# Kernel tuning notes

Measured on AMD Instinct MI355X. Metric: run time of the kernel, lower is better.

Reference implementation:

```python
import jax, jax.numpy as jnp
import numpy as np

N = 100000   # nodes
E = 3200000  # edges
M = 4096     # moves
K = 16       # orders per move
NEG_SLOPE = 0.2  # PyG GATv2Conv default negative_slope

PARAM_SHAPES = {
    'g1_Wl': (10, 15), 'g1_Wr': (10, 15), 'g1_att': (10,), 'g1_b': (10,),
    'g2_Wl': (10, 25), 'g2_Wr': (10, 25), 'g2_att': (10,), 'g2_b': (10,),
    'g3_Wl': (10, 25), 'g3_Wr': (10, 25), 'g3_att': (10,), 'g3_b': (10,),
    'vt_W': (20, 29), 'vt_b': (20,), 'va_W': (1, 20), 'va_b': (1,),
    'vv_W': (10, 20), 'vv_b': (10,), 'vl_W': (1, 10), 'vl_b': (1,),
    'at_W': (20, 48), 'at_b': (20,), 'dt_W': (20, 23), 'dt_b': (20,),
    'oa_W': (1, 20), 'oa_b': (1,), 'ov_W': (1, 20), 'ov_b': (1,),
}
PARAM_NAMES = list(PARAM_SHAPES.keys())


def _linear(x, W, b):
    return x @ W.T + b


def _gatv2(x, src, dst, Wl, Wr, att, b):
    # GATv2Conv (heads=1, self-loops appended by caller), eval mode (no dropout)
    xl = x @ Wl.T  # messages from source nodes
    xr = x @ Wr.T
    e = (jax.nn.leaky_relu(xl[src] + xr[dst], NEG_SLOPE) * att).sum(-1)  # [E+N]
    emax = jax.ops.segment_max(e, dst, num_segments=N)
    ee = jnp.exp(e - emax[dst])
    denom = jax.ops.segment_sum(ee, dst, num_segments=N)
    alpha = ee / denom[dst]
    return jax.ops.segment_sum(alpha[:, None] * xl[src], dst, num_segments=N) + b


def _forward(x1, x2, edges, move_src, move_dst, move_armies, is_attack, params):
    (g1_Wl, g1_Wr, g1_att, g1_b,
     g2_Wl, g2_Wr, g2_att, g2_b,
     g3_Wl, g3_Wr, g3_att, g3_b,
     vt_W, vt_b, va_W, va_b, vv_W, vv_b, vl_W, vl_b,
     at_W, at_b, dt_W, dt_b, oa_W, oa_b, ov_W, ov_b) = params
    x2t = jnp.tile(x2, (N, 1))  # [N,4]
    self_idx = jnp.arange(N, dtype=edges.dtype)
    src = jnp.concatenate([edges[0], self_idx])
    dst = jnp.concatenate([edges[1], self_idx])
    x = jax.nn.relu(_gatv2(x1, src, dst, g1_Wl, g1_Wr, g1_att, g1_b))
    x = jax.nn.relu(_gatv2(jnp.concatenate([x, x1], 1), src, dst, g2_Wl, g2_Wr, g2_att, g2_b))
    x = jax.nn.relu(_gatv2(jnp.concatenate([x, x1], 1), src, dst, g3_Wl, g3_Wr, g3_att, g3_b))  # [N,10]
    # per-move order tensors (vectorized over [M,K]); deploy uses move_src as target
    xs, xd = x[move_src], x[move_dst]       # [M,K,10]
    x1s, x1d = x1[move_src], x1[move_dst]   # [M,K,15]
    extra = 0.6 * move_armies - 0.7 * (x1d[..., 3] + x1d[..., 4])
    attack_in = jnp.concatenate([xs, xd, x1s[..., 3:], x1d[..., 1:],
                                 move_armies[..., None], extra[..., None]], -1)  # [M,K,48]
    deploy_in = jnp.concatenate([xs, x1s[..., 3:], move_armies[..., None]], -1)  # [M,K,23]
    feat = jnp.where(is_attack[..., None] == 1,
                     _linear(attack_in, at_W, at_b),
                     _linear(deploy_in, dt_W, dt_b))
    feat = jax.nn.relu(feat)  # dropout = identity (eval)
    attn = jax.nn.softmax(_linear(feat, oa_W, oa_b), axis=1)  # softmax over orders
    p = (attn * _linear(feat, ov_W, ov_b)).sum(axis=(1, 2))   # [M]
    # value head: attention pooling over all nodes
    Vn = jax.nn.relu(_linear(jnp.concatenate([x, x1, x2t], 1), vt_W, vt_b))  # [N,20]
    vatt = jax.nn.softmax(_linear(Vn, va_W, va_b), axis=0)
    Vp = jax.nn.relu((vatt * _linear(Vn, vv_W, vv_b)).sum(axis=0))
    V = jnp.tanh(_linear(Vp, vl_W, vl_b))[0]
    return V, jax.nn.log_softmax(p, axis=0)


def setup_inputs() -> dict:
    key = jax.random.key(0)
    ks = iter(jax.random.split(key, 64))
    inp = {
        'x1': jax.random.normal(next(ks), (N, 15), jnp.float32),
        'x2': jax.random.normal(next(ks), (4,), jnp.float32),
        'edges': jax.random.randint(next(ks), (2, E), 0, N, jnp.int32),
        'move_src': jax.random.randint(next(ks), (M, K), 0, N, jnp.int32),
        'move_dst': jax.random.randint(next(ks), (M, K), 0, N, jnp.int32),
        'move_armies': jax.random.uniform(next(ks), (M, K), jnp.float32) * 10.0,
        'is_attack': jax.random.randint(next(ks), (M, K), 0, 2, jnp.int32),
    }
    for name, shape in PARAM_SHAPES.items():
        inp[name] = jax.random.normal(next(ks), shape, jnp.float32) * 0.1
    return inp


def reference(x1, x2, edges, move_src, move_dst, move_armies, is_attack,
              g1_Wl, g1_Wr, g1_att, g1_b, g2_Wl, g2_Wr, g2_att, g2_b,
              g3_Wl, g3_Wr, g3_att, g3_b, vt_W, vt_b, va_W, va_b,
              vv_W, vv_b, vl_W, vl_b, at_W, at_b, dt_W, dt_b,
              oa_W, oa_b, ov_W, ov_b):
    params = (g1_Wl, g1_Wr, g1_att, g1_b, g2_Wl, g2_Wr, g2_att, g2_b,
              g3_Wl, g3_Wr, g3_att, g3_b, vt_W, vt_b, va_W, va_b,
              vv_W, vv_b, vl_W, vl_b, at_W, at_b, dt_W, dt_b,
              oa_W, oa_b, ov_W, ov_b)
    return _forward(x1, x2, edges, move_src, move_dst, move_armies, is_attack, params)
```

## Files before the change

### kernel.cpp

```cpp
#include <hip/hip_runtime.h>
#include <hip/hip_fp16.h>
#include <math.h>

#define NN 100000
#define NE 3200000
#define MM 4096
#define KK 16
#define NEG_SLOPE 0.2f
#define SUB 8
#define BSH 8
#define NB 391
#define PCH 4096
#define FCAP 9728
#define XS 12
#define XSU 4
#define PART_BLOCKS ((NE + NN + PCH - 1) / PCH)
#define LIN_BLOCKS  ((NN + 255) / 256)
#define MOVE_BLOCKS ((MM * KK) / 256)
#define VAL_BLOCKS  ((NN + 255) / 256)
#define CSTR 16
#define PZ ((int)0xAAAAAAAAu)

typedef float vfloat2 __attribute__((__vector_size__(2 * sizeof(float))));

__device__ __forceinline__ void f8x10_decode(const uint4& w, float* xs) {
    vfloat2 f0 = __builtin_amdgcn_cvt_pk_f32_fp8(w.x, false); xs[0]=f0[0]; xs[1]=f0[1];
    vfloat2 f1 = __builtin_amdgcn_cvt_pk_f32_fp8(w.x, true);  xs[2]=f1[0]; xs[3]=f1[1];
    vfloat2 f2 = __builtin_amdgcn_cvt_pk_f32_fp8(w.y, false); xs[4]=f2[0]; xs[5]=f2[1];
    vfloat2 f3 = __builtin_amdgcn_cvt_pk_f32_fp8(w.y, true);  xs[6]=f3[0]; xs[7]=f3[1];
    vfloat2 f4 = __builtin_amdgcn_cvt_pk_f32_fp8(w.z, false); xs[8]=f4[0]; xs[9]=f4[1];
}
__device__ __forceinline__ uint4 f8x10_encode(const float* v) {
    unsigned u0 = __builtin_amdgcn_cvt_pk_fp8_f32(v[0], v[1], 0, false);
    u0 = __builtin_amdgcn_cvt_pk_fp8_f32(v[2], v[3], u0, true);
    unsigned u1 = __builtin_amdgcn_cvt_pk_fp8_f32(v[4], v[5], 0, false);
    u1 = __builtin_amdgcn_cvt_pk_fp8_f32(v[6], v[7], u1, true);
    unsigned u2 = __builtin_amdgcn_cvt_pk_fp8_f32(v[8], v[9], 0, false);
    return make_uint4(u0, u1, u2, 0u);
}

__global__ __launch_bounds__(256) void part_lin1_kernel(const int* __restrict__ edges,
                                                        int* __restrict__ cnt,
                                                        unsigned* __restrict__ recs,
                                                        const float* __restrict__ x1,
                                                        const float* __restrict__ Wl,
                                                        const float* __restrict__ Wr,
                                                        unsigned* __restrict__ xl8,
                                                        float* __restrict__ xr) {
    int t = threadIdx.x;
    if (blockIdx.x >= PART_BLOCKS) {
        int i = (blockIdx.x - PART_BLOCKS) * 256 + t;
        if (i >= NN) return;
        float in[15];
        #pragma unroll
        for (int j = 0; j < 15; j++) in[j] = x1[(long)i * 15 + j];
        float sl[10];
        #pragma unroll
        for (int o = 0; o < 10; o++) {
            float l = 0.f, r = 0.f;
            #pragma unroll
            for (int j = 0; j < 15; j++) {
                l += Wl[o * 15 + j] * in[j];
                r += Wr[o * 15 + j] * in[j];
            }
            sl[o] = l;
            xr[(long)i * XS + o] = r;
        }
        *(uint4*)(xl8 + (long)i * XSU) = f8x10_encode(sl);
        return;
    }
    __shared__ unsigned rl[PCH];
    __shared__ unsigned short bb[PCH];
    __shared__ int h[NB];
    __shared__ int gb[NB];
    __shared__ int cur[NB];
    const int total = NE + NN;
    int base = blockIdx.x * PCH;
    int n = min(PCH, total - base);
    for (int b = t; b < NB; b += 256) { h[b] = 0; cur[b] = 0; }
    __syncthreads();
    for (int j = t; j < n; j += 256) {
        int i = base + j;
        int s, d;
        if (i < NE) { s = edges[i]; d = edges[NE + i]; }
        else        { s = i - NE; d = s; }
        rl[j] = ((unsigned)(d & 255) << 17) | (unsigned)s;
        int b = d >> BSH;
        bb[j] = (unsigned short)b;
        atomicAdd(&h[b], 1);
    }
    __syncthreads();
    for (int b = t; b < NB; b += 256) {
        int hv = h[b];
        if (hv > 0) gb[b] = atomicAdd(&cnt[b * CSTR], hv) - PZ;
    }
    __syncthreads();
    for (int j = t; j < n; j += 256) {
        int b = bb[j];
        int l = atomicAdd(&cur[b], 1);
        int pos = gb[b] + l;
        if (pos >= 0 && pos < FCAP) recs[(long)b * FCAP + pos] = rl[j];
    }
}

__global__ __launch_bounds__(1024) void fine_sort_kernel(const unsigned* __restrict__ recs,
                                                         const int* __restrict__ cnt,
                                                         int* __restrict__ csr_src,
                                                         int* __restrict__ offsets) {
    __shared__ unsigned rl[FCAP];
    __shared__ int scn[512];
    __shared__ int hist[256];
    __shared__ int sc[256];
    __shared__ int hb[257];
    __shared__ int cur[256];
    int b = blockIdx.x;
    int t = threadIdx.x;
    int c = 0;
    if (t < 512) {
        c = (t < NB) ? min(max(cnt[t * CSTR] - PZ, 0), FCAP) : 0;
        scn[t] = c;
    }
    __syncthreads();
    for (int off = 1; off < 512; off <<= 1) {
        int v = 0;
        if (t < 512 && t >= off) v = scn[t - off];
        __syncthreads();
        if (t < 512) scn[t] += v;
        __syncthreads();
    }
    int beg = (b == 0) ? 0 : scn[b - 1];
    int nb = min(max(cnt[b * CSTR] - PZ, 0), FCAP);
    int nodebase = b << BSH;
    int nnodes = min(256, NN - nodebase);
    if (t < 256) { hist[t] = 0; cur[t] = 0; }
    __syncthreads();
    const unsigned* rsrc = recs + (long)b * FCAP;
    for (int j = t; j < nb; j += 1024) {
        unsigned r = rsrc[j];
        rl[j] = r;
        atomicAdd(&hist[r >> 17], 1);
    }
    __syncthreads();
    int hv = (t < 256) ? hist[t] : 0;
    if (t < 256) sc[t] = hv;
    __syncthreads();
    for (int off = 1; off < 256; off <<= 1) {
        int v = 0;
        if (t < 256 && t >= off) v = sc[t - off];
        __syncthreads();
        if (t < 256) sc[t] += v;
        __syncthreads();
    }
    if (t < 256) hb[t] = sc[t] - hv;
    if (t == 0) hb[256] = nb;
    __syncthreads();
    for (int j = t; j < nb; j += 1024) {
        unsigned r = rl[j];
        int l = r >> 17;
        int p = hb[l] + atomicAdd(&cur[l], 1);
        csr_src[beg + p] = (int)(r & 0x1FFFFu);
    }
    if (t < nnodes) offsets[nodebase + t] = beg + hb[t];
    if (b == NB - 1 && t == 0) offsets[NN] = beg + nb;
}

template<bool FUSE_NEXT>
__global__ void gat_aggregate_kernel(const int* __restrict__ csr_src,
                                     const int* __restrict__ offsets,
                                     const unsigned* __restrict__ xl8,
                                     const float* __restrict__ xr,
                                     const float* __restrict__ att,
                                     const float* __restrict__ b,
                                     const float* __restrict__ x1,
                                     const float* __restrict__ nWl,
                                     const float* __restrict__ nWr,
                                     unsigned* __restrict__ xlo,
                                     float* __restrict__ xro,
                                     float* __restrict__ xout)
{
    int t = blockIdx.x * blockDim.x + threadIdx.x;
    int node = t / SUB;
    int lane = t % SUB;
    if (node >= NN) return;
    float xrn[12], a[10];
    const float4* xr4 = (const float4*)(xr + (long)node * XS);
    #pragma unroll
    for (int q = 0; q < 3; q++) {
        float4 v = xr4[q];
        xrn[4*q] = v.x; xrn[4*q+1] = v.y; xrn[4*q+2] = v.z; xrn[4*q+3] = v.w;
    }
    #pragma unroll
    for (int h = 0; h < 10; h++) a[h] = att[h];
    int beg = offsets[node], end = offsets[node + 1];
    float den = 0.f, num[10];
    #pragma unroll
    for (int h = 0; h < 10; h++) num[h] = 0.f;
    int j = beg + lane;
    for (; j + 3 * SUB < end; j += 4 * SUB) {
        int s0 = csr_src[j];
        int s1 = csr_src[j + SUB];
        int s2 = csr_src[j + 2 * SUB];
        int s3 = csr_src[j + 3 * SUB];
        uint4 wa[4];
        wa[0] = *(const uint4*)(xl8 + (long)s0 * XSU);
        wa[1] = *(const uint4*)(xl8 + (long)s1 * XSU);
        wa[2] = *(const uint4*)(xl8 + (long)s2 * XSU);
        wa[3] = *(const uint4*)(xl8 + (long)s3 * XSU);
        #pragma unroll
        for (int q = 0; q < 4; q++) {
            float xs[10];
            f8x10_decode(wa[q], xs);
            float e = 0.f;
            #pragma unroll
            for (int h = 0; h < 10; h++) {
                float v = xs[h] + xrn[h];
                v = (v >= 0.f) ? v : NEG_SLOPE * v;
                e += v * a[h];
            }
            float w = __expf(e);
            den += w;
            #pragma unroll
            for (int h = 0; h < 10; h++) num[h] += w * xs[h];
        }
    }
    for (; j < end; j += SUB) {
        int s = csr_src[j];
        uint4 wa = *(const uint4*)(xl8 + (long)s * XSU);
        float xs[10];
        f8x10_decode(wa, xs);
        float e = 0.f;
        #pragma unroll
        for (int h = 0; h < 10; h++) {
            float v = xs[h] + xrn[h];
            v = (v >= 0.f) ? v : NEG_SLOPE * v;
            e += v * a[h];
        }
        float w = __expf(e);
        den += w;
        #pragma unroll
        for (int h = 0; h < 10; h++) num[h] += w * xs[h];
    }
    #pragma unroll
    for (int off = SUB / 2; off; off >>= 1) {
        den += __shfl_xor(den, off, SUB);
        #pragma unroll
        for (int h = 0; h < 10; h++) num[h] += __shfl_xor(num[h], off, SUB);
    }
    float inv = 1.f / den;
    float xo[10];
    #pragma unroll
    for (int h = 0; h < 10; h++) xo[h] = fmaxf(num[h] * inv + b[h], 0.f);
    if (FUSE_NEXT) {
        if (lane < 5) {
            float in2[25];
            #pragma unroll
            for (int h = 0; h < 10; h++) in2[h] = xo[h];
            #pragma unroll
            for (int h = 0; h < 15; h++) in2[10 + h] = x1[(long)node * 15 + h];
            int o0 = 2 * lane, o1 = 2 * lane + 1;
            float sl0 = 0.f, sl1 = 0.f, sr0 = 0.f, sr1 = 0.f;
            #pragma unroll
            for (int jj = 0; jj < 25; jj++) {
                sl0 += nWl[o0 * 25 + jj] * in2[jj];
                sl1 += nWl[o1 * 25 + jj] * in2[jj];
                sr0 += nWr[o0 * 25 + jj] * in2[jj];
                sr1 += nWr[o1 * 25 + jj] * in2[jj];
            }
            unsigned pk = __builtin_amdgcn_cvt_pk_fp8_f32(sl0, sl1, 0, false);
            ((unsigned short*)(xlo + (long)node * XSU))[lane] = (unsigned short)pk;
            *(float2*)(xro + (long)node * XS + o0) = make_float2(sr0, sr1);
        }
    } else {
        if (lane == 0) {
            #pragma unroll
            for (int h = 0; h < 10; h++) xout[(long)node * XS + h] = xo[h];
        }
    }
}

__global__ void move_value_kernel(const float* __restrict__ x,
                                  const float* __restrict__ x1,
                                  const float* __restrict__ x2,
                                  const int* __restrict__ msrc,
                                  const int* __restrict__ mdst,
                                  const float* __restrict__ armies,
                                  const int* __restrict__ isatk,
                                  const float* __restrict__ at_W, const float* __restrict__ at_b,
                                  const float* __restrict__ dt_W, const float* __restrict__ dt_b,
                                  const float* __restrict__ oa_W, const float* __restrict__ oa_b,
                                  const float* __restrict__ ov_W, const float* __restrict__ ov_b,
                                  const float* __restrict__ vt_W, const float* __restrict__ vt_b,
                                  const float* __restrict__ va_W, const float* __restrict__ va_b,
                                  const float* __restrict__ vv_W, const float* __restrict__ vv_b,
                                  float* __restrict__ p,
                                  float* __restrict__ partials) {
    if (blockIdx.x < MOVE_BLOCKS) {
        int t = blockIdx.x * 256 + threadIdx.x;
        int m = t >> 4;
        int k = t & 15;
        int s = msrc[t], d = mdst[t];
        float arm = armies[t];
        bool atk = (isatk[t] == 1);
        float xsrc[12];
        const float4* xs4 = (const float4*)(x + (long)s * XS);
        #pragma unroll
        for (int q = 0; q < 3; q++) {
            float4 v = xs4[q];
            xsrc[4*q]=v.x; xsrc[4*q+1]=v.y; xsrc[4*q+2]=v.z; xsrc[4*q+3]=v.w;
        }
        float feat[20];
        if (atk) {
            float in[48];
            #pragma unroll
            for (int h = 0; h < 10; h++) in[h] = xsrc[h];
            const float4* xd4 = (const float4*)(x + (long)d * XS);
            float xdst[12];
            #pragma unroll
            for (int q = 0; q < 3; q++) {
                float4 v = xd4[q];
                xdst[4*q]=v.x; xdst[4*q+1]=v.y; xdst[4*q+2]=v.z; xdst[4*q+3]=v.w;
            }
            #pragma unroll
            for (int h = 0; h < 10; h++) in[10 + h] = xdst[h];
            #pragma unroll
            for (int h = 0; h < 12; h++) in[20 + h] = x1[(long)s * 15 + 3 + h];
            #pragma unroll
            for (int h = 0; h < 14; h++) in[32 + h] = x1[(long)d * 15 + 1 + h];
            in[46] = arm;
            in[47] = 0.6f * arm - 0.7f * (x1[(long)d * 15 + 3] + x1[(long)d * 15 + 4]);
            #pragma unroll
            for (int o = 0; o < 20; o++) {
                float sum = at_b[o];
                #pragma unroll
                for (int j = 0; j < 48; j++) sum += at_W[o * 48 + j] * in[j];
                feat[o] = fmaxf(sum, 0.f);
            }
        } else {
            float in[23];
            #pragma unroll
            for (int h = 0; h < 10; h++) in[h] = xsrc[h];
            #pragma unroll
            for (int h = 0; h < 12; h++) in[10 + h] = x1[(long)s * 15 + 3 + h];
            in[22] = arm;
            #pragma unroll
            for (int o = 0; o < 20; o++) {
                float sum = dt_b[o];
                #pragma unroll
                for (int j = 0; j < 23; j++) sum += dt_W[o * 23 + j] * in[j];
                feat[o] = fmaxf(sum, 0.f);
            }
        }
        float oa = oa_b[0], ov = ov_b[0];
        #pragma unroll
        for (int j = 0; j < 20; j++) {
            oa += oa_W[j] * feat[j];
            ov += ov_W[j] * feat[j];
        }
        float mx = oa;
        #pragma unroll
        for (int off = 8; off; off >>= 1) mx = fmaxf(mx, __shfl_xor(mx, off, 16));
        float w = __expf(oa - mx);
        float nume = w * ov;
        float den = w;
        #pragma unroll
        for (int off = 8; off; off >>= 1) {
            nume += __shfl_xor(nume, off, 16);
            den  += __shfl_xor(den,  off, 16);
        }
        if (k == 0) p[m] = nume / den;
        return;
    }
    __shared__ float sm[4][11];
    int vb = blockIdx.x - MOVE_BLOCKS;
    int i = vb * 256 + threadIdx.x;
    float w = 0.f;
    float acc[10];
    #pragma unroll
    for (int h = 0; h < 10; h++) acc[h] = 0.f;
    if (i < NN) {
        float in[29];
        const float4* xi4 = (const float4*)(x + (long)i * XS);
        float xi[12];
        #pragma unroll
        for (int q = 0; q < 3; q++) {
            float4 v = xi4[q];
            xi[4*q]=v.x; xi[4*q+1]=v.y; xi[4*q+2]=v.z; xi[4*q+3]=v.w;
        }
        #pragma unroll
        for (int h = 0; h < 10; h++) in[h] = xi[h];
        #pragma unroll
        for (int h = 0; h < 15; h++) in[10 + h] = x1[(long)i * 15 + h];
        #pragma unroll
        for (int h = 0; h < 4; h++) in[25 + h] = x2[h];
        float Vn[20];
        #pragma unroll
        for (int o = 0; o < 20; o++) {
            float s = vt_b[o];
            #pragma unroll
            for (int j = 0; j < 29; j++) s += vt_W[o * 29 + j] * in[j];
            Vn[o] = fmaxf(s, 0.f);
        }
        float lg = va_b[0];
        #pragma unroll
        for (int j = 0; j < 20; j++) lg += va_W[j] * Vn[j];
        w = __expf(lg);
        #pragma unroll
        for (int o = 0; o < 10; o++) {
            float s = vv_b[o];
            #pragma unroll
            for (int j = 0; j < 20; j++) s += vv_W[o * 20 + j] * Vn[j];
            acc[o] = w * s;
        }
    }
    #pragma unroll
    for (int off = 32; off; off >>= 1) {
        w += __shfl_xor(w, off, 64);
        #pragma unroll
        for (int h = 0; h < 10; h++) acc[h] += __shfl_xor(acc[h], off, 64);
    }
    int wid = threadIdx.x >> 6;
    if ((threadIdx.x & 63) == 0) {
        #pragma unroll
        for (int h = 0; h < 10; h++) sm[wid][h] = acc[h];
        sm[wid][10] = w;
    }
    __syncthreads();
    if (threadIdx.x < 11) {
        int c = threadIdx.x;
        partials[(long)vb * 12 + c] = sm[0][c] + sm[1][c] + sm[2][c] + sm[3][c];
    }
}

__global__ void final_kernel(const float* __restrict__ p,
                             const float* __restrict__ partials,
                             const float* __restrict__ vl_W, const float* __restrict__ vl_b,
                             float* __restrict__ out) {
    if (blockIdx.x == 0) {
        __shared__ float sm[256];
        int tid = threadIdx.x;
        float mx = -INFINITY;
        for (int i = tid; i < MM; i += 256) mx = fmaxf(mx, p[i]);
        sm[tid] = mx; __syncthreads();
        for (int s = 128; s; s >>= 1) { if (tid < s) sm[tid] = fmaxf(sm[tid], sm[tid + s]); __syncthreads(); }
        mx = sm[0]; __syncthreads();
        float sum = 0.f;
        for (int i = tid; i < MM; i += 256) sum += expf(p[i] - mx);
        sm[tid] = sum; __syncthreads();
        for (int s = 128; s; s >>= 1) { if (tid < s) sm[tid] += sm[tid + s]; __syncthreads(); }
        float ls = mx + logf(sm[0]);
        for (int i = tid; i < MM; i += 256) out[1 + i] = p[i] - ls;
    } else if (threadIdx.x < 64) {
        int lane = threadIdx.x;
        float s[11];
        #pragma unroll
        for (int c = 0; c < 11; c++) s[c] = 0.f;
        for (int j = lane; j < VAL_BLOCKS; j += 64)
            #pragma unroll
            for (int c = 0; c < 11; c++) s[c] += partials[(long)j * 12 + c];
        #pragma unroll
        for (int off = 32; off; off >>= 1)
            #pragma unroll
            for (int c = 0; c < 11; c++) s[c] += __shfl_xor(s[c], off, 64);
        if (lane == 0) {
            float inv = 1.0f / s[10];
            float v = vl_b[0];
            #pragma unroll
            for (int h = 0; h < 10; h++) v += vl_W[h] * fmaxf(s[h] * inv, 0.f);
            out[0] = tanhf(v);
        }
    }
}

extern "C" void kernel_launch(void* const* d_in, const int* in_sizes, int n_in,
                              void* d_out, int out_size, void* d_ws, size_t ws_size,
                              hipStream_t stream) {
    const float* x1      = (const float*)d_in[0];
    const float* x2      = (const float*)d_in[1];
    const int*   edges   = (const int*)d_in[2];
    const int*   msrc    = (const int*)d_in[3];
    const int*   mdst    = (const int*)d_in[4];
    const float* armies  = (const float*)d_in[5];
    const int*   isatk   = (const int*)d_in[6];
    const float* g1_Wl = (const float*)d_in[7],  *g1_Wr = (const float*)d_in[8];
    const float* g1_att= (const float*)d_in[9],  *g1_b  = (const float*)d_in[10];
    const float* g2_Wl = (const float*)d_in[11], *g2_Wr = (const float*)d_in[12];
    const float* g2_att= (const float*)d_in[13], *g2_b  = (const float*)d_in[14];
    const float* g3_Wl = (const float*)d_in[15], *g3_Wr = (const float*)d_in[16];
    const float* g3_att= (const float*)d_in[17], *g3_b  = (const float*)d_in[18];
    const float* vt_W  = (const float*)d_in[19], *vt_b  = (const float*)d_in[20];
    const float* va_W  = (const float*)d_in[21], *va_b  = (const float*)d_in[22];
    const float* vv_W  = (const float*)d_in[23], *vv_b  = (const float*)d_in[24];
    const float* vl_W  = (const float*)d_in[25], *vl_b  = (const float*)d_in[26];
    const float* at_W  = (const float*)d_in[27], *at_b  = (const float*)d_in[28];
    const float* dt_W  = (const float*)d_in[29], *dt_b  = (const float*)d_in[30];
    const float* oa_W  = (const float*)d_in[31], *oa_b  = (const float*)d_in[32];
    const float* ov_W  = (const float*)d_in[33], *ov_b  = (const float*)d_in[34];

    float* out = (float*)d_out;

    float* ws = (float*)d_ws;
    unsigned* xl8A = (unsigned*)ws;
    unsigned* xl8B = xl8A + (long)NN * XSU;
    float* xrA = (float*)(xl8B + (long)NN * XSU);
    float* xrB = xrA + (long)NN * XS;
    float* xF  = xrB + (long)NN * XS;
    int* csr_src = (int*)(xF + (long)NN * XS);
    int* offsets = csr_src + (NE + NN);
    unsigned* recs = (unsigned*)(offsets + NN + 4);
    int* cnt   = (int*)(recs + (long)NB * FCAP);
    float* pbuf = (float*)(cnt + NB * CSTR + 16);
    float* partials = pbuf + MM;

    const int aggBlocks = ((long)NN * SUB + 255) / 256;

    part_lin1_kernel<<<PART_BLOCKS + LIN_BLOCKS, 256, 0, stream>>>(
        edges, cnt, recs, x1, g1_Wl, g1_Wr, xl8A, xrA);
    fine_sort_kernel<<<NB, 1024, 0, stream>>>(recs, cnt, csr_src, offsets);
    gat_aggregate_kernel<true><<<aggBlocks, 256, 0, stream>>>(
        csr_src, offsets, xl8A, xrA, g1_att, g1_b, x1, g2_Wl, g2_Wr, xl8B, xrB, nullptr);
    gat_aggregate_kernel<true><<<aggBlocks, 256, 0, stream>>>(
        csr_src, offsets, xl8B, xrB, g2_att, g2_b, x1, g3_Wl, g3_Wr, xl8A, xrA, nullptr);
    gat_aggregate_kernel<false><<<aggBlocks, 256, 0, stream>>>(
        csr_src, offsets, xl8A, xrA, g3_att, g3_b, x1, nullptr, nullptr, nullptr, nullptr, xF);
    move_value_kernel<<<MOVE_BLOCKS + VAL_BLOCKS, 256, 0, stream>>>(
        xF, x1, x2, msrc, mdst, armies, isatk,
        at_W, at_b, dt_W, dt_b, oa_W, oa_b, ov_W, ov_b,
        vt_W, vt_b, va_W, va_b, vv_W, vv_b, pbuf, partials);
    final_kernel<<<2, 256, 0, stream>>>(pbuf, partials, vl_W, vl_b, out);
}
```

Before: 334.8 us.

## Split coarse bucket partition into count, scan, and scatter kernels

Replaces the single-pass partition, which claimed bucket slots with global atomics and staged records in shared memory, with three kernels: a per-chunk histogram, a per-bucket scan over chunk histograms, and a scatter that re-reads edges and writes records at deterministic offsets. This removes global atomic contention on the bucket counters and the large shared-memory staging, which should raise occupancy. In exchange the edge array is read twice and two extra launches are added. The chunk size is doubled and the histogram buffer reuses the csr_src region.

```diff
diff --git a/kernel.cpp b/kernel.cpp
--- a/kernel.cpp
+++ b/kernel.cpp
@@ -10,11 +10,11 @@
 #define SUB 8
 #define BSH 8
 #define NB 391
-#define PCH 4096
+#define PCH 8192
 #define FCAP 9728
 #define XS 12
 #define XSU 4
-#define PART_BLOCKS ((NE + NN + PCH - 1) / PCH)
+#define CNT_BLOCKS ((NE + NN + PCH - 1) / PCH)
 #define LIN_BLOCKS  ((NN + 255) / 256)
 #define MOVE_BLOCKS ((MM * KK) / 256)
 #define VAL_BLOCKS  ((NN + 255) / 256)
@@ -40,16 +40,15 @@
 }
 
 __global__ __launch_bounds__(256) void part_lin1_kernel(const int* __restrict__ edges,
-                                                        int* __restrict__ cnt,
-                                                        unsigned* __restrict__ recs,
+                                                        int* __restrict__ hist,
                                                         const float* __restrict__ x1,
                                                         const float* __restrict__ Wl,
                                                         const float* __restrict__ Wr,
                                                         unsigned* __restrict__ xl8,
                                                         float* __restrict__ xr) {
     int t = threadIdx.x;
-    if (blockIdx.x >= PART_BLOCKS) {
-        int i = (blockIdx.x - PART_BLOCKS) * 256 + t;
+    if (blockIdx.x >= CNT_BLOCKS) {
+        int i = (blockIdx.x - CNT_BLOCKS) * 256 + t;
         if (i >= NN) return;
         float in[15];
         #pragma unroll
@@ -69,37 +68,65 @@
         *(uint4*)(xl8 + (long)i * XSU) = f8x10_encode(sl);
         return;
     }
-    __shared__ unsigned rl[PCH];
-    __shared__ unsigned short bb[PCH];
     __shared__ int h[NB];
-    __shared__ int gb[NB];
-    __shared__ int cur[NB];
     const int total = NE + NN;
     int base = blockIdx.x * PCH;
     int n = min(PCH, total - base);
-    for (int b = t; b < NB; b += 256) { h[b] = 0; cur[b] = 0; }
+    for (int b = t; b < NB; b += 256) h[b] = 0;
+    __syncthreads();
+    for (int j = t; j < n; j += 256) {
+        int i = base + j;
+        int d = (i < NE) ? edges[NE + i] : (i - NE);
+        atomicAdd(&h[d >> BSH], 1);
+    }
+    __syncthreads();
+    for (int b = t; b < NB; b += 256) hist[blockIdx.x * NB + b] = h[b];
+}
+
+__global__ __launch_bounds__(64) void scan_kernel(int* __restrict__ hist,
+                                                  int* __restrict__ cnt) {
+    int b = blockIdx.x;
+    int lane = threadIdx.x;
+    int base = 0;
+    const int chunks = (CNT_BLOCKS + 63) / 64;
+    for (int c = 0; c < chunks; c++) {
+        int idx = c * 64 + lane;
+        int v = (idx < CNT_BLOCKS) ? hist[idx * NB + b] : 0;
+        int x = v;
+        #pragma unroll
+        for (int off = 1; off < 64; off <<= 1) {
+            int y = __shfl_up(x, off, 64);
+            if (lane >= off) x += y;
+        }
+        if (idx < CNT_BLOCKS) hist[idx * NB + b] = base + x - v;
+        base += __shfl(x, 63, 64);
+    }
+    if (lane == 0) cnt[b * CSTR] = base + PZ;
+}
+
+__global__ __launch_bounds__(256) void scatter_kernel(const int* __restrict__ edges,
+                                                      const int* __restrict__ hist,
+                                                      unsigned* __restrict__ recs) {
+    __shared__ int gb[NB];
+    __shared__ int cur[NB];
+    int t = threadIdx.x;
+    const int total = NE + NN;
+    int base = blockIdx.x * PCH;
+    int n = min(PCH, total - base);
+    for (int b = t; b < NB; b += 256) {
+        gb[b] = hist[blockIdx.x * NB + b];
+        cur[b] = 0;
+    }
     __syncthreads();
     for (int j = t; j < n; j += 256) {
         int i = base + j;
         int s, d;
         if (i < NE) { s = edges[i]; d = edges[NE + i]; }
         else        { s = i - NE; d = s; }
-        rl[j] = ((unsigned)(d & 255) << 17) | (unsigned)s;
         int b = d >> BSH;
-        bb[j] = (unsigned short)b;
-        atomicAdd(&h[b], 1);
-    }
-    __syncthreads();
-    for (int b = t; b < NB; b += 256) {
-        int hv = h[b];
-        if (hv > 0) gb[b] = atomicAdd(&cnt[b * CSTR], hv) - PZ;
-    }
-    __syncthreads();
-    for (int j = t; j < n; j += 256) {
-        int b = bb[j];
         int l = atomicAdd(&cur[b], 1);
         int pos = gb[b] + l;
-        if (pos >= 0 && pos < FCAP) recs[(long)b * FCAP + pos] = rl[j];
+        if (pos < FCAP) recs[(long)b * FCAP + pos] = ((unsigned)(d & 255) << 17) | (unsigned)s;
     }
 }
 
@@ -510,11 +537,14 @@
     int* cnt   = (int*)(recs + (long)NB * FCAP);
     float* pbuf = (float*)(cnt + NB * CSTR + 16);
     float* partials = pbuf + MM;
+    int* hist = csr_src;
 
     const int aggBlocks = ((long)NN * SUB + 255) / 256;
 
-    part_lin1_kernel<<<PART_BLOCKS + LIN_BLOCKS, 256, 0, stream>>>(
-        edges, cnt, recs, x1, g1_Wl, g1_Wr, xl8A, xrA);
+    part_lin1_kernel<<<CNT_BLOCKS + LIN_BLOCKS, 256, 0, stream>>>(
+        edges, hist, x1, g1_Wl, g1_Wr, xl8A, xrA);
+    scan_kernel<<<NB, 64, 0, stream>>>(hist, cnt);
+    scatter_kernel<<<CNT_BLOCKS, 256, 0, stream>>>(edges, hist, recs);
     fine_sort_kernel<<<NB, 1024, 0, stream>>>(recs, cnt, csr_src, offsets);
     gat_aggregate_kernel<true><<<aggBlocks, 256, 0, stream>>>(
         csr_src, offsets, xl8A, xrA, g1_att, g1_b, x1, g2_Wl, g2_Wr, xl8B, xrB, nullptr);
```

Result: slower. 344.9 us (+3.0%).

## Replace two-level bucket sort CSR build with global histogram, scan, atomic scatter

Applied to the files above, without the earlier changes.

Builds the destination-sorted CSR with a global per-node atomic histogram, a two-kernel prefix scan and an atomic-cursor scatter of sources. This replaces the coarse bucket partition plus shared-memory fine sort. The goal is to drop the intermediate record buffer and the large-LDS fine-sort kernel. In exchange it adds two extra launches and many global atomics on random destinations. Within a node the edge order becomes nondeterministic, which may change floating-point summation order.

```diff
diff --git a/kernel.cpp b/kernel.cpp
--- a/kernel.cpp
+++ b/kernel.cpp
@@ -8,17 +8,14 @@
 #define KK 16
 #define NEG_SLOPE 0.2f
 #define SUB 8
-#define BSH 8
 #define NB 391
-#define PCH 4096
-#define FCAP 9728
 #define XS 12
 #define XSU 4
-#define PART_BLOCKS ((NE + NN + PCH - 1) / PCH)
+#define HIST_BLOCKS 512
 #define LIN_BLOCKS  ((NN + 255) / 256)
+#define SC_BLOCKS   1024
 #define MOVE_BLOCKS ((MM * KK) / 256)
 #define VAL_BLOCKS  ((NN + 255) / 256)
-#define CSTR 16
 #define PZ ((int)0xAAAAAAAAu)
 
 typedef float vfloat2 __attribute__((__vector_size__(2 * sizeof(float))));
@@ -40,16 +37,15 @@
 }
 
 __global__ __launch_bounds__(256) void part_lin1_kernel(const int* __restrict__ edges,
-                                                        int* __restrict__ cnt,
-                                                        unsigned* __restrict__ recs,
+                                                        int* __restrict__ ghist,
                                                         const float* __restrict__ x1,
                                                         const float* __restrict__ Wl,
                                                         const float* __restrict__ Wr,
                                                         unsigned* __restrict__ xl8,
                                                         float* __restrict__ xr) {
     int t = threadIdx.x;
-    if (blockIdx.x >= PART_BLOCKS) {
-        int i = (blockIdx.x - PART_BLOCKS) * 256 + t;
+    if (blockIdx.x >= HIST_BLOCKS) {
+        int i = (blockIdx.x - HIST_BLOCKS) * 256 + t;
         if (i >= NN) return;
         float in[15];
         #pragma unroll
@@ -69,99 +65,87 @@
         *(uint4*)(xl8 + (long)i * XSU) = f8x10_encode(sl);
         return;
     }
-    __shared__ unsigned rl[PCH];
-    __shared__ unsigned short bb[PCH];
-    __shared__ int h[NB];
-    __shared__ int gb[NB];
-    __shared__ int cur[NB];
-    const int total = NE + NN;
-    int base = blockIdx.x * PCH;
-    int n = min(PCH, total - base);
-    for (int b = t; b < NB; b += 256) { h[b] = 0; cur[b] = 0; }
+    long gid = (long)blockIdx.x * 256 + t;
+    const long stride = (long)HIST_BLOCKS * 256;
+    for (long i = gid; i < NE; i += stride)
+        atomicAdd(&ghist[edges[NE + i]], 1);
+}
+
+__global__ __launch_bounds__(256) void scan1_kernel(const int* __restrict__ ghist,
+                                                    int* __restrict__ chunkTot) {
+    int c = blockIdx.x, t = threadIdx.x;
+    int i = c * 256 + t;
+    int w = (i < NN) ? (ghist[i] - PZ + 1) : 0;
+    #pragma unroll
+    for (int off = 32; off; off >>= 1) w += __shfl_xor(w, off, 64);
+    __shared__ int rb[4];
+    if ((t & 63) == 0) rb[t >> 6] = w;
     __syncthreads();
-    for (int j = t; j < n; j += 256) {
-        int i = base + j;
-        int s, d;
-        if (i < NE) { s = edges[i]; d = edges[NE + i]; }
-        else        { s = i - NE; d = s; }
-        rl[j] = ((unsigned)(d & 255) << 17) | (unsigned)s;
-        int b = d >> BSH;
-        bb[j] = (unsigned short)b;
-        atomicAdd(&h[b], 1);
-    }
+    if (t == 0) chunkTot[c] = rb[0] + rb[1] + rb[2] + rb[3];
+}
+
+__global__ __launch_bounds__(256) void scan2_kernel(const int* __restrict__ ghist,
+                                                    const int* __restrict__ chunkTot,
+                                                    int* __restrict__ offsets,
+                                                    int* __restrict__ cur,
+                                                    int* __restrict__ csr_src) {
+    __shared__ int sTot[NB];
+    __shared__ int rb[4];
+    __shared__ int wt[4];
+    int c = blockIdx.x, t = threadIdx.x;
+    int lane = t & 63, wid = t >> 6;
+    for (int j = t; j < NB; j += 256) sTot[j] = chunkTot[j];
     __syncthreads();
-    for (int b = t; b < NB; b += 256) {
-        int hv = h[b];
-        if (hv > 0) gb[b] = atomicAdd(&cnt[b * CSTR], hv) - PZ;
-    }
+    int part = 0;
+    for (int j = t; j < c; j += 256) part += sTot[j];
+    #pragma unroll
+    for (int off = 32; off; off >>= 1) part += __shfl_xor(part, off, 64);
+    if (lane == 0) rb[wid] = part;
     __syncthreads();
-    for (int j = t; j < n; j += 256) {
-        int b = bb[j];
-        int l = atomicAdd(&cur[b], 1);
-        int pos = gb[b] + l;
-        if (pos >= 0 && pos < FCAP) recs[(long)b * FCAP + pos] = rl[j];
-    }
-}
-
-__global__ __launch_bounds__(1024) void fine_sort_kernel(const unsigned* __restrict__ recs,
-                                                         const int* __restrict__ cnt,
-                                                         int* __restrict__ csr_src,
-                                                         int* __restrict__ offsets) {
-    __shared__ unsigned rl[FCAP];
-    __shared__ int scn[512];
-    __shared__ int hist[256];
-    __shared__ int sc[256];
-    __shared__ int hb[257];
-    __shared__ int cur[256];
-    int b = blockIdx.x;
-    int t = threadIdx.x;
-    int c = 0;
-    if (t < 512) {
-        c = (t < NB) ? min(max(cnt[t * CSTR] - PZ, 0), FCAP) : 0;
-        scn[t] = c;
-    }
+    int base = rb[0] + rb[1] + rb[2] + rb[3];
+    int i = c * 256 + t;
+    int w = (i < NN) ? (ghist[i] - PZ + 1) : 0;
+    int x = w;
+    #pragma unroll
+    for (int off = 1; off < 64; off <<= 1) {
+        int y = __shfl_up(x, off, 64);
+        if (lane >= off) x += y;
+    }
+    if (lane == 63) wt[wid] = x;
     __syncthreads();
-    for (int off = 1; off < 512; off <<= 1) {
-        int v = 0;
-        if (t < 512 && t >= off) v = scn[t - off];
-        __syncthreads();
-        if (t < 512) scn[t] += v;
-        __syncthreads();
-    }
-    int beg = (b == 0) ? 0 : scn[b - 1];
-    int nb = min(max(cnt[b * CSTR] - PZ, 0), FCAP);
-    int nodebase = b << BSH;
-    int nnodes = min(256, NN - nodebase);
-    if (t < 256) { hist[t] = 0; cur[t] = 0; }
-    __syncthreads();
-    const unsigned* rsrc = recs + (long)b * FCAP;
-    for (int j = t; j < nb; j += 1024) {
-        unsigned r = rsrc[j];
-        rl[j] = r;
-        atomicAdd(&hist[r >> 17], 1);
-    }
-    __syncthreads();
-    int hv = (t < 256) ? hist[t] : 0;
-    if (t < 256) sc[t] = hv;
-    __syncthreads();
-    for (int off = 1; off < 256; off <<= 1) {
-        int v = 0;
-        if (t < 256 && t >= off) v = sc[t - off];
-        __syncthreads();
-        if (t < 256) sc[t] += v;
-        __syncthreads();
-    }
-    if (t < 256) hb[t] = sc[t] - hv;
-    if (t == 0) hb[256] = nb;
-    __syncthreads();
-    for (int j = t; j < nb; j += 1024) {
-        unsigned r = rl[j];
-        int l = r >> 17;
-        int p = hb[l] + atomicAdd(&cur[l], 1);
-        csr_src[beg + p] = (int)(r & 0x1FFFFu);
-    }
-    if (t < nnodes) offsets[nodebase + t] = beg + hb[t];
-    if (b == NB - 1 && t == 0) offsets[NN] = beg + nb;
+    int wb = 0;
+    for (int q = 0; q < wid; q++) wb += wt[q];
+    int endp = base + wb + x;
+    if (i < NN) {
+        int beg = endp - w;
+        offsets[i] = beg;
+        cur[i] = beg;
+        csr_src[endp - 1] = i;
+        if (i == NN - 1) offsets[NN] = endp;
+    }
+}
+
+__global__ __launch_bounds__(256) void scatter_kernel(const int* __restrict__ edges,
+                                                      int* __restrict__ cur,
+                                                      int* __restrict__ csr_src) {
+    long gid = (long)blockIdx.x * 256 + threadIdx.x;
+    const long stride = (long)SC_BLOCKS * 256;
+    for (long i0 = gid; i0 < NE; i0 += 4 * stride) {
+        int ss[4], dd[4], pp[4];
+        bool vl[4];
+        #pragma unroll
+        for (int q = 0; q < 4; q++) {
+            long i = i0 + q * stride;
+            vl[q] = (i < NE);
+            if (vl[q]) { ss[q] = edges[i]; dd[q] = edges[NE + i]; }
+        }
+        #pragma unroll
+        for (int q = 0; q < 4; q++)
+            if (vl[q]) pp[q] = atomicAdd(&cur[dd[q]], 1);
+        #pragma unroll
+        for (int q = 0; q < 4; q++)
+            if (vl[q]) csr_src[pp[q]] = ss[q];
+    }
 }
 
 template<bool FUSE_NEXT>
@@ -506,16 +490,19 @@
     float* xF  = xrB + (long)NN * XS;
     int* csr_src = (int*)(xF + (long)NN * XS);
     int* offsets = csr_src + (NE + NN);
-    unsigned* recs = (unsigned*)(offsets + NN + 4);
-    int* cnt   = (int*)(recs + (long)NB * FCAP);
-    float* pbuf = (float*)(cnt + NB * CSTR + 16);
+    int* ghist   = offsets + NN + 4;
+    int* cur     = ghist + NN;
+    int* chunkTot= cur + NN;
+    float* pbuf = (float*)(chunkTot + NB + 9);
     float* partials = pbuf + MM;
 
     const int aggBlocks = ((long)NN * SUB + 255) / 256;
 
-    part_lin1_kernel<<<PART_BLOCKS + LIN_BLOCKS, 256, 0, stream>>>(
-        edges, cnt, recs, x1, g1_Wl, g1_Wr, xl8A, xrA);
-    fine_sort_kernel<<<NB, 1024, 0, stream>>>(recs, cnt, csr_src, offsets);
+    part_lin1_kernel<<<HIST_BLOCKS + LIN_BLOCKS, 256, 0, stream>>>(
+        edges, ghist, x1, g1_Wl, g1_Wr, xl8A, xrA);
+    scan1_kernel<<<NB, 256, 0, stream>>>(ghist, chunkTot);
+    scan2_kernel<<<NB, 256, 0, stream>>>(ghist, chunkTot, offsets, cur, csr_src);
+    scatter_kernel<<<SC_BLOCKS, 256, 0, stream>>>(edges, cur, csr_src);
     gat_aggregate_kernel<true><<<aggBlocks, 256, 0, stream>>>(
         csr_src, offsets, xl8A, xrA, g1_att, g1_b, x1, g2_Wl, g2_Wr, xl8B, xrB, nullptr);
     gat_aggregate_kernel<true><<<aggBlocks, 256, 0, stream>>>(
```

Result: slower. 678.1 us (+102.5%).

## Locally sort edge records in shared memory before coalesced global scatter

Applied to the files above, without the earlier changes.

The partition kernel now builds a bucket histogram and prefix scan first, then places records into a shared-memory buffer sorted by bucket. Each bucket's records can then be written to global memory as contiguous runs instead of scattered stores. The fine sort kernel likewise scatters into shared memory and then writes csr_src sequentially for coalesced stores, re-reading records from global memory instead of caching them in LDS. The cost is an extra pass reading the edges array, an extra scan, and more barriers.

```diff
diff --git a/kernel.cpp b/kernel.cpp
--- a/kernel.cpp
+++ b/kernel.cpp
@@ -69,37 +69,56 @@
         *(uint4*)(xl8 + (long)i * XSU) = f8x10_encode(sl);
         return;
     }
-    __shared__ unsigned rl[PCH];
-    __shared__ unsigned short bb[PCH];
+    __shared__ unsigned srt[PCH];
+    __shared__ unsigned short sbk[PCH];
+    __shared__ int scn[512];
     __shared__ int h[NB];
     __shared__ int gb[NB];
     __shared__ int cur[NB];
+    __shared__ int lb[NB];
     const int total = NE + NN;
     int base = blockIdx.x * PCH;
     int n = min(PCH, total - base);
     for (int b = t; b < NB; b += 256) { h[b] = 0; cur[b] = 0; }
+    __syncthreads();
+    for (int j = t; j < n; j += 256) {
+        int i = base + j;
+        int d = (i < NE) ? edges[NE + i] : (i - NE);
+        atomicAdd(&h[d >> BSH], 1);
+    }
+    __syncthreads();
+    for (int b = t; b < NB; b += 256) {
+        int hv = h[b];
+        if (hv > 0) gb[b] = atomicAdd(&cnt[b * CSTR], hv) - PZ;
+    }
+    scn[t]       = (t < NB)       ? h[t]       : 0;
+    scn[t + 256] = (t + 256 < NB) ? h[t + 256] : 0;
+    __syncthreads();
+    for (int off = 1; off < 512; off <<= 1) {
+        int v0 = (t >= off)       ? scn[t - off]       : 0;
+        int v1 = (t + 256 >= off) ? scn[t + 256 - off] : 0;
+        __syncthreads();
+        scn[t] += v0; scn[t + 256] += v1;
+        __syncthreads();
+    }
+    if (t < NB)       lb[t]       = scn[t]       - h[t];
+    if (t + 256 < NB) lb[t + 256] = scn[t + 256] - h[t + 256];
     __syncthreads();
     for (int j = t; j < n; j += 256) {
         int i = base + j;
         int s, d;
         if (i < NE) { s = edges[i]; d = edges[NE + i]; }
         else        { s = i - NE; d = s; }
-        rl[j] = ((unsigned)(d & 255) << 17) | (unsigned)s;
         int b = d >> BSH;
-        bb[j] = (unsigned short)b;
-        atomicAdd(&h[b], 1);
-    }
-    __syncthreads();
-    for (int b = t; b < NB; b += 256) {
-        int hv = h[b];
-        if (hv > 0) gb[b] = atomicAdd(&cnt[b * CSTR], hv) - PZ;
+        int slot = lb[b] + atomicAdd(&cur[b], 1);
+        srt[slot] = ((unsigned)(d & 255) << 17) | (unsigned)s;
+        sbk[slot] = (unsigned short)b;
     }
     __syncthreads();
     for (int j = t; j < n; j += 256) {
-        int b = bb[j];
-        int l = atomicAdd(&cur[b], 1);
-        int pos = gb[b] + l;
-        if (pos >= 0 && pos < FCAP) recs[(long)b * FCAP + pos] = rl[j];
+        int b = sbk[j];
+        int gpos = gb[b] + (j - lb[b]);
+        if (gpos >= 0 && gpos < FCAP) recs[(long)b * FCAP + gpos] = srt[j];
     }
 }
 
@@ -107,7 +126,7 @@
                                                          const int* __restrict__ cnt,
                                                          int* __restrict__ csr_src,
                                                          int* __restrict__ offsets) {
-    __shared__ unsigned rl[FCAP];
+    __shared__ unsigned srt2[FCAP];
     __shared__ int scn[512];
     __shared__ int hist[256];
     __shared__ int sc[256];
@@ -135,11 +154,8 @@
     if (t < 256) { hist[t] = 0; cur[t] = 0; }
     __syncthreads();
     const unsigned* rsrc = recs + (long)b * FCAP;
-    for (int j = t; j < nb; j += 1024) {
-        unsigned r = rsrc[j];
-        rl[j] = r;
-        atomicAdd(&hist[r >> 17], 1);
-    }
+    for (int j = t; j < nb; j += 1024)
+        atomicAdd(&hist[rsrc[j] >> 17], 1);
     __syncthreads();
     int hv = (t < 256) ? hist[t] : 0;
     if (t < 256) sc[t] = hv;
@@ -155,11 +171,14 @@
     if (t == 0) hb[256] = nb;
     __syncthreads();
     for (int j = t; j < nb; j += 1024) {
-        unsigned r = rl[j];
+        unsigned r = rsrc[j];
         int l = r >> 17;
         int p = hb[l] + atomicAdd(&cur[l], 1);
-        csr_src[beg + p] = (int)(r & 0x1FFFFu);
-    }
+        srt2[p] = r & 0x1FFFFu;
+    }
+    __syncthreads();
+    for (int j = t; j < nb; j += 1024)
+        csr_src[beg + j] = (int)srt2[j];
     if (t < nnodes) offsets[nodebase + t] = beg + hb[t];
     if (b == NB - 1 && t == 0) offsets[NN] = beg + nb;
 }
```

Measured after the change: 325.1 us. 1.03x faster.
